# Optimization experiments

Hardware: AMD Instinct MI355X
Metric: run time of the kernel (lower is better)

## Reference

```python
import jax, jax.numpy as jnp
import numpy as np

B, S, D, H = 2, 2048, 1024, 16
DH = D // H  # 64
EPS = 1e-5


def setup_inputs() -> dict:
    key = jax.random.key(0)
    ks = jax.random.split(key, 16)
    s = 0.02
    return {
        "emb": jax.random.normal(ks[0], (B, S, D), dtype=jnp.float32),
        # per-head projections, stacked: torch Linear weight layout [out, in] -> [H, DH, D]
        "Wq": jax.random.normal(ks[1], (H, DH, D), dtype=jnp.float32) * s,
        "bq": jnp.zeros((H, DH), dtype=jnp.float32),
        "Wk": jax.random.normal(ks[2], (H, DH, D), dtype=jnp.float32) * s,
        "bk": jnp.zeros((H, DH), dtype=jnp.float32),
        "Wv": jax.random.normal(ks[3], (H, DH, D), dtype=jnp.float32) * s,
        "bv": jnp.zeros((H, DH), dtype=jnp.float32),
        "W0": jax.random.normal(ks[4], (D, D), dtype=jnp.float32) * s,
        "b0": jnp.zeros((D,), dtype=jnp.float32),
        "g1": jnp.ones((D,), dtype=jnp.float32),
        "be1": jnp.zeros((D,), dtype=jnp.float32),
        "W1": jax.random.normal(ks[5], (4 * D, D), dtype=jnp.float32) * s,
        "b1": jnp.zeros((4 * D,), dtype=jnp.float32),
        "W2": jax.random.normal(ks[6], (D, 4 * D), dtype=jnp.float32) * s,
        "b2": jnp.zeros((D,), dtype=jnp.float32),
        "g2": jnp.ones((D,), dtype=jnp.float32),
        "be2": jnp.zeros((D,), dtype=jnp.float32),
    }


def _layer_norm(x, g, b):
    mu = jnp.mean(x, axis=-1, keepdims=True)
    var = jnp.mean(jnp.square(x - mu), axis=-1, keepdims=True)
    return (x - mu) * jax.lax.rsqrt(var + EPS) * g + b


def reference(emb, Wq, bq, Wk, bk, Wv, bv, W0, b0, g1, be1, W1, b1, W2, b2, g2, be2):
    # per-head Q/K/V projections, batched over heads  -> [B, H, S, DH]
    q = jnp.einsum("bsd,hed->bhse", emb, Wq) + bq[None, :, None, :]
    k = jnp.einsum("bsd,hed->bhse", emb, Wk) + bk[None, :, None, :]
    v = jnp.einsum("bsd,hed->bhse", emb, Wv) + bv[None, :, None, :]
    # NOTE: original module applies NO scale before softmax; it divides the
    # softmax(QK^T) @ V output by sqrt(d_head) afterwards. Kept faithfully.
    scores = jnp.einsum("bhse,bhte->bhst", q, k)  # [B,H,S,S]
    attn = jax.nn.softmax(scores, axis=-1)
    z = jnp.einsum("bhst,bhte->bhse", attn, v) / np.sqrt(DH).astype(np.float32)
    # concat heads along feature dim (head 0 first) -> [B, S, D]
    z = z.transpose(0, 2, 1, 3).reshape(B, S, D)
    z = z @ W0.T + b0
    out1 = _layer_norm(z + emb, g1, be1)
    h = jax.nn.relu(out1 @ W1.T + b1)  # [B, S, 4D]
    out2 = _layer_norm(out1 + (h @ W2.T + b2), g2, be2)
    return out2
```

## Files before the change

kernel.cpp:

```cpp
#include <hip/hip_runtime.h>
#include <hip/hip_bf16.h>
#include <cstdint>
#include <cmath>

#define DEV __device__ __forceinline__

typedef float f32x4 __attribute__((ext_vector_type(4)));
typedef float f32x16 __attribute__((ext_vector_type(16)));
typedef __bf16 bf16x8 __attribute__((ext_vector_type(8)));
typedef unsigned short u16;
typedef u16 u16x8 __attribute__((ext_vector_type(8)));
typedef u16 u16x4 __attribute__((ext_vector_type(4)));

DEV u16 f2bf(float f) {
  union { float f; uint32_t u; } x{f};
  uint32_t r = x.u + 0x7FFFu + ((x.u >> 16) & 1u);
  return (u16)(r >> 16);
}

DEV void gl_lds16(const u16* g, u16* l) {
  __builtin_amdgcn_global_load_lds((const __attribute__((address_space(1))) void*)g,
                                   (__attribute__((address_space(3))) void*)l, 16, 0, 0);
}

__global__ __launch_bounds__(256) void k_cvt_all(
    const float* __restrict__ emb, const float* __restrict__ Wq,
    const float* __restrict__ Wk, const float* __restrict__ Wv,
    const float* __restrict__ W0, const float* __restrict__ W1,
    const float* __restrict__ W2,
    u16* __restrict__ embb, u16* __restrict__ Wqb, u16* __restrict__ Wkb,
    u16* __restrict__ Wvb, u16* __restrict__ W0b, u16* __restrict__ W1b,
    u16* __restrict__ W2b) {
  const int step = gridDim.x * blockDim.x;
  for (int i4 = blockIdx.x * blockDim.x + threadIdx.x; i4 < 4194304; i4 += step) {
    const int i = i4 * 4;
    const float* s; u16* d; int off;
    if (i < 4194304)       { s = emb; d = embb; off = 0; }
    else if (i < 5242880)  { s = Wq;  d = Wqb;  off = 4194304; }
    else if (i < 6291456)  { s = Wk;  d = Wkb;  off = 5242880; }
    else if (i < 7340032)  { s = Wv;  d = Wvb;  off = 6291456; }
    else if (i < 8388608)  { s = W0;  d = W0b;  off = 7340032; }
    else if (i < 12582912) { s = W1;  d = W1b;  off = 8388608; }
    else                   { s = W2;  d = W2b;  off = 12582912; }
    float4 v = *reinterpret_cast<const float4*>(s + (i - off));
    u16x4 o;
    o[0] = f2bf(v.x); o[1] = f2bf(v.y); o[2] = f2bf(v.z); o[3] = f2bf(v.w);
    *reinterpret_cast<u16x4*>(d + (i - off)) = o;
  }
}


template <int MODE>
DEV void gemm_core128(const u16* __restrict__ A, const u16* __restrict__ B,
                      const float* __restrict__ bias, const float* __restrict__ res,
                      void* __restrict__ C, int N, int K, int m0, int n0,
                      float oscale) {
  __shared__ u16 sA[2][128 * 32];
  __shared__ u16 sB[2][128 * 32];
  const int tid = threadIdx.x;
  const int w = tid >> 6, l = tid & 63;
  const int lr = l & 15, lg = l >> 4;
  const int wr = (w >> 1) * 64, wc = (w & 1) * 64;

  f32x4 acc[4][4] = {};

  const int nt = K >> 5;
  const int sr = w * 16 + (l >> 2);
  const int sc = (l & 3) * 8;

  auto stage = [&](int buf, int t) {
    const u16* ga = A + (size_t)(m0 + sr) * K + t * 32 + sc;
    const u16* gb = B + (size_t)(n0 + sr) * K + t * 32 + sc;
    gl_lds16(ga, &sA[buf][w * 512]);
    gl_lds16(ga + (size_t)64 * K, &sA[buf][2048 + w * 512]);
    gl_lds16(gb, &sB[buf][w * 512]);
    gl_lds16(gb + (size_t)64 * K, &sB[buf][2048 + w * 512]);
  };

  auto compute = [&](int buf) {
    bf16x8 af[4], bfr[4];
#pragma unroll
    for (int mf = 0; mf < 4; ++mf)
      af[mf] = *(const bf16x8*)&sA[buf][(wr + mf * 16 + lr) * 32 + lg * 8];
#pragma unroll
    for (int nf = 0; nf < 4; ++nf)
      bfr[nf] = *(const bf16x8*)&sB[buf][(wc + nf * 16 + lr) * 32 + lg * 8];
#pragma unroll
    for (int mf = 0; mf < 4; ++mf)
#pragma unroll
      for (int nf = 0; nf < 4; ++nf)
        acc[mf][nf] = __builtin_amdgcn_mfma_f32_16x16x32_bf16(af[mf], bfr[nf],
                                                              acc[mf][nf], 0, 0, 0);
  };

  stage(0, 0);
  __syncthreads();
  int cur = 0;
  for (int t = 0; t < nt - 1; ++t) {
    stage(cur ^ 1, t + 1);
    compute(cur);
    __syncthreads();
    cur ^= 1;
  }
  compute(cur);

#pragma unroll
  for (int nf = 0; nf < 4; ++nf) {
    const int col = n0 + wc + nf * 16 + lr;
    const float bv = bias[col];
#pragma unroll
    for (int mf = 0; mf < 4; ++mf) {
      const int row0 = m0 + wr + mf * 16 + lg * 4;
#pragma unroll
      for (int r = 0; r < 4; ++r) {
        float v = acc[mf][nf][r] + bv;
        if (MODE == 0) v *= oscale;
        if (MODE == 1) v = fmaxf(v, 0.0f);
        const size_t idx = (size_t)(row0 + r) * N + col;
        if (MODE == 2) ((float*)C)[idx] = v + res[idx];
        else ((u16*)C)[idx] = f2bf(v);
      }
    }
  }
}

template <int MODE>
DEV void gemm_core64(const u16* __restrict__ A, const u16* __restrict__ B,
                     const float* __restrict__ bias, const float* __restrict__ res,
                     void* __restrict__ C, int N, int K, int m0, int n0,
                     float oscale) {
  __shared__ u16 sA[2][64 * 32];
  __shared__ u16 sB[2][128 * 32];
  const int tid = threadIdx.x;
  const int w = tid >> 6, l = tid & 63;
  const int lr = l & 15, lg = l >> 4;
  const int wr = (w >> 1) * 32, wc = (w & 1) * 64;

  f32x4 acc[2][4] = {};

  const int nt = K >> 5;
  const int sr = w * 16 + (l >> 2);
  const int sc = (l & 3) * 8;

  auto stage = [&](int buf, int t) {
    gl_lds16(A + (size_t)(m0 + sr) * K + t * 32 + sc, &sA[buf][w * 512]);
    const u16* gb = B + (size_t)(n0 + sr) * K + t * 32 + sc;
    gl_lds16(gb, &sB[buf][w * 512]);
    gl_lds16(gb + (size_t)64 * K, &sB[buf][2048 + w * 512]);
  };

  auto compute = [&](int buf) {
    bf16x8 af[2], bfr[4];
#pragma unroll
    for (int mf = 0; mf < 2; ++mf)
      af[mf] = *(const bf16x8*)&sA[buf][(wr + mf * 16 + lr) * 32 + lg * 8];
#pragma unroll
    for (int nf = 0; nf < 4; ++nf)
      bfr[nf] = *(const bf16x8*)&sB[buf][(wc + nf * 16 + lr) * 32 + lg * 8];
#pragma unroll
    for (int mf = 0; mf < 2; ++mf)
#pragma unroll
      for (int nf = 0; nf < 4; ++nf)
        acc[mf][nf] = __builtin_amdgcn_mfma_f32_16x16x32_bf16(af[mf], bfr[nf],
                                                              acc[mf][nf], 0, 0, 0);
  };

  stage(0, 0);
  __syncthreads();
  int cur = 0;
  for (int t = 0; t < nt - 1; ++t) {
    stage(cur ^ 1, t + 1);
    compute(cur);
    __syncthreads();
    cur ^= 1;
  }
  compute(cur);

#pragma unroll
  for (int nf = 0; nf < 4; ++nf) {
    const int col = n0 + wc + nf * 16 + lr;
    const float bv = bias[col];
#pragma unroll
    for (int mf = 0; mf < 2; ++mf) {
      const int row0 = m0 + wr + mf * 16 + lg * 4;
#pragma unroll
      for (int r = 0; r < 4; ++r) {
        float v = acc[mf][nf][r] + bv;
        if (MODE == 0) v *= oscale;
        if (MODE == 1) v = fmaxf(v, 0.0f);
        const size_t idx = (size_t)(row0 + r) * N + col;
        if (MODE == 2) ((float*)C)[idx] = v + res[idx];
        else ((u16*)C)[idx] = f2bf(v);
      }
    }
  }
}

template <int MODE>
__global__ __launch_bounds__(256) void k_gemm(const u16* __restrict__ A,
                                              const u16* __restrict__ B,
                                              const float* __restrict__ bias,
                                              const float* __restrict__ res,
                                              void* __restrict__ C, int N, int K) {
  gemm_core128<MODE>(A, B, bias, res, C, N, K, blockIdx.x * 128, blockIdx.y * 128, 1.0f);
}

template <int MODE>
__global__ __launch_bounds__(256) void k_gemm64(const u16* __restrict__ A,
                                                const u16* __restrict__ B,
                                                const float* __restrict__ bias,
                                                const float* __restrict__ res,
                                                void* __restrict__ C, int N, int K) {
  gemm_core64<MODE>(A, B, bias, res, C, N, K, blockIdx.x * 64, blockIdx.y * 128, 1.0f);
}

__global__ __launch_bounds__(256) void k_gemm_qkv(
    const u16* __restrict__ A, const u16* __restrict__ B0, const u16* __restrict__ B1,
    const u16* __restrict__ B2, const float* __restrict__ c0,
    const float* __restrict__ c1, const float* __restrict__ c2,
    u16* __restrict__ O0, u16* __restrict__ O1, u16* __restrict__ O2) {
  const int z = blockIdx.z;
  const u16* B = (z == 0) ? B0 : (z == 1) ? B1 : B2;
  const float* bias = (z == 0) ? c0 : (z == 1) ? c1 : c2;
  u16* O = (z == 0) ? O0 : (z == 1) ? O1 : O2;
  const float sc = (z == 0) ? 1.44269504f : 1.0f;
  gemm_core64<0>(A, B, bias, nullptr, O, 1024, 1024, blockIdx.x * 64,
                 blockIdx.y * 128, sc);
}

__global__ __launch_bounds__(256, 4) void k_attn(const u16* __restrict__ Q,
                                                 const u16* __restrict__ K,
                                                 const u16* __restrict__ V,
                                                 float* __restrict__ pz,
                                                 float* __restrict__ pl) {
  const int id = blockIdx.x;
  const int virt = (id & 7) * 128 + (id >> 3);
  const int bh = virt >> 5;
  const int qt = (virt >> 1) & 15;
  const int half = virt & 1;
  const int b = bh >> 4, h = bh & 15;
  const int tid = threadIdx.x;
  const int w = tid >> 6, l = tid & 63;
  const int q32 = l & 31, hi = l >> 5;

  __shared__ u16 Kl[2][4096];
  __shared__ u16 VT[2][4096];

  const size_t rb = (size_t)b * 2048;
  const int c0 = h * 64;
  const int q0w = qt * 128 + w * 32;
  const int t0 = half * 16;

  bf16x8 qb[4];
#pragma unroll
  for (int st = 0; st < 4; ++st)
    qb[st] = *(const bf16x8*)(Q + (rb + q0w + q32) * 1024 + c0 + st * 16 + hi * 8);

  f32x16 zacc[2] = {};
  f32x4 lacc = {};

  const int skv = w * 16 + (l >> 3);
  const int sc8 = l & 7;
  auto stage_k = [&](int pp, int t) {
#pragma unroll
    for (int cq = 0; cq < 2; ++cq) {
      const int kvl = skv + cq * 8;
      const int dh0 = (sc8 ^ (kvl & 7)) * 8;
      gl_lds16(K + (rb + t * 64 + kvl) * 1024 + c0 + dh0,
               &Kl[pp][w * 1024 + cq * 512]);
    }
  };

  const int vp = tid & 31, vd0 = (tid >> 5) * 8;
  u16x8 va0, va1;
  auto vload = [&](int t) {
    const u16* v0 = V + (rb + t * 64 + 2 * vp) * 1024 + c0 + vd0;
    va0 = *(const u16x8*)v0;
    va1 = *(const u16x8*)(v0 + 1024);
  };
  auto vstore = [&](int pp) {
#pragma unroll
    for (int i = 0; i < 8; ++i) {
      const int dh = vd0 + i;
      const int off = ((2 * vp) & 7) + 8 * ((vp >> 2) ^ (dh & 7));
      uint32_t pk = (uint32_t)va0[i] | ((uint32_t)va1[i] << 16);
      *(uint32_t*)&VT[pp][dh * 64 + off] = pk;
    }
  };

  stage_k(0, t0);
  vload(t0);
  vstore(0);
  __syncthreads();

  for (int tt = 0; tt < 16; ++tt) {
    const int bp = tt & 1;
    if (tt + 1 < 16) {
      stage_k(bp ^ 1, t0 + tt + 1);
      vload(t0 + tt + 1);
    }
    f32x16 s[2] = {};
    __builtin_amdgcn_s_setprio(1);
#pragma unroll
    for (int nf = 0; nf < 2; ++nf)
#pragma unroll
      for (int st = 0; st < 4; ++st) {
        bf16x8 ka = *(const bf16x8*)&Kl[bp][(nf * 32 + q32) * 64 +
                                            ((st * 2 + hi) ^ (q32 & 7)) * 8];
        s[nf] = __builtin_amdgcn_mfma_f32_32x32x16_bf16(ka, qb[st], s[nf], 0, 0, 0);
      }
    __builtin_amdgcn_s_setprio(0);

    uint32_t c[16];
#pragma unroll
    for (int nf = 0; nf < 2; ++nf)
#pragma unroll
      for (int m2 = 0; m2 < 8; ++m2) {
        float p0 = exp2f(s[nf][2 * m2]);
        float p1 = exp2f(s[nf][2 * m2 + 1]);
        lacc[m2 & 3] += p0 + p1;
        uint32_t pk;
        asm("v_cvt_pk_bf16_f32 %0, %1, %2" : "=v"(pk) : "v"(p0), "v"(p1));
        c[nf * 8 + m2] = pk;
      }
#pragma unroll
    for (int ks = 0; ks < 4; ++ks) {
      asm("v_permlane32_swap_b32 %0, %1" : "+v"(c[4 * ks]), "+v"(c[4 * ks + 2]));
      asm("v_permlane32_swap_b32 %0, %1" : "+v"(c[4 * ks + 1]), "+v"(c[4 * ks + 3]));
    }

    if (tt + 1 < 16) vstore(bp ^ 1);

    __builtin_amdgcn_s_setprio(1);
#pragma unroll
    for (int ks = 0; ks < 4; ++ks) {
      union { uint32_t u[4]; bf16x8 v; } pa;
#pragma unroll
      for (int i = 0; i < 4; ++i) pa.u[i] = c[4 * ks + i];
#pragma unroll
      for (int nd = 0; nd < 2; ++nd) {
        bf16x8 vb = *(const bf16x8*)&VT[bp][(nd * 32 + q32) * 64 +
                                            ((ks * 2 + hi) ^ (q32 & 7)) * 8];
        zacc[nd] = __builtin_amdgcn_mfma_f32_32x32x16_bf16(pa.v, vb, zacc[nd], 0, 0, 0);
      }
    }
    __builtin_amdgcn_s_setprio(0);
    __syncthreads();
  }

  float* pzb = pz + (size_t)virt * 8192;
#pragma unroll
  for (int r = 0; r < 16; ++r) {
    const int crow = (r & 3) + 8 * (r >> 2) + 4 * hi;
#pragma unroll
    for (int nd = 0; nd < 2; ++nd)
      pzb[(w * 32 + crow) * 64 + nd * 32 + q32] = zacc[nd][r];
  }
  float lrun = (lacc[0] + lacc[1]) + (lacc[2] + lacc[3]);
  float ltot = lrun + __shfl_xor(lrun, 32, 64);
  if (hi == 0) pl[virt * 128 + w * 32 + q32] = ltot;
}

__global__ __launch_bounds__(256) void k_attn_merge(const float* __restrict__ pz,
                                                    const float* __restrict__ pl,
                                                    u16* __restrict__ Z) {
  const int id = blockIdx.x;
  const int virt2 = (id & 7) * 64 + (id >> 3);
  const int bh = virt2 >> 4, qt = virt2 & 15;
  const int b = bh >> 4, h = bh & 15;
  const int va = 2 * virt2;
  const int tid = threadIdx.x;
  const int row = tid >> 1;
  const int col0 = (tid & 1) * 32;

  const float la = pl[va * 128 + row];
  const float lb = pl[(va + 1) * 128 + row];
  const float inv = 0.125f / (la + lb);

  const float* za = pz + (size_t)va * 8192 + row * 64 + col0;
  const float* zb = za + 8192;
  u16* zo = Z + ((size_t)b * 2048 + qt * 128 + row) * 1024 + h * 64 + col0;
#pragma unroll
  for (int e = 0; e < 8; ++e) {
    float4 a = *(const float4*)(za + e * 4);
    float4 bv = *(const float4*)(zb + e * 4);
    u16x4 o;
    o[0] = f2bf((a.x + bv.x) * inv);
    o[1] = f2bf((a.y + bv.y) * inv);
    o[2] = f2bf((a.z + bv.z) * inv);
    o[3] = f2bf((a.w + bv.w) * inv);
    *(u16x4*)(zo + e * 4) = o;
  }
}

template <bool WBF>
__global__ __launch_bounds__(256) void k_ln(const float* __restrict__ x,
                                            const float* __restrict__ g,
                                            const float* __restrict__ be,
                                            float* __restrict__ of,
                                            u16* __restrict__ ob) {
  const int row = blockIdx.x;
  const int tid = threadIdx.x;
  const float* xr = x + (size_t)row * 1024;
  float4 v = *(const float4*)(xr + tid * 4);
  float s = v.x + v.y + v.z + v.w;
  float s2 = v.x * v.x + v.y * v.y + v.z * v.z + v.w * v.w;
#pragma unroll
  for (int st = 1; st < 64; st <<= 1) {
    s += __shfl_xor(s, st, 64);
    s2 += __shfl_xor(s2, st, 64);
  }
  __shared__ float ps[8];
  if ((tid & 63) == 0) { ps[tid >> 6] = s; ps[4 + (tid >> 6)] = s2; }
  __syncthreads();
  s = ps[0] + ps[1] + ps[2] + ps[3];
  s2 = ps[4] + ps[5] + ps[6] + ps[7];
  const float mu = s * 0.0009765625f;
  const float var = s2 * 0.0009765625f - mu * mu;
  const float rs = rsqrtf(var + 1e-5f);
  float4 gg = *(const float4*)(g + tid * 4);
  float4 bb = *(const float4*)(be + tid * 4);
  float4 o;
  o.x = (v.x - mu) * rs * gg.x + bb.x;
  o.y = (v.y - mu) * rs * gg.y + bb.y;
  o.z = (v.z - mu) * rs * gg.z + bb.z;
  o.w = (v.w - mu) * rs * gg.w + bb.w;
  *(float4*)(of + (size_t)row * 1024 + tid * 4) = o;
  if (WBF) {
    u16x4 q;
    q[0] = f2bf(o.x); q[1] = f2bf(o.y); q[2] = f2bf(o.z); q[3] = f2bf(o.w);
    *(u16x4*)(ob + (size_t)row * 1024 + tid * 4) = q;
  }
}

extern "C" void kernel_launch(void* const* d_in, const int* in_sizes, int n_in,
                              void* d_out, int out_size, void* d_ws, size_t ws_size,
                              hipStream_t stream) {
  const float* emb = (const float*)d_in[0];
  const float* Wq  = (const float*)d_in[1];
  const float* bq  = (const float*)d_in[2];
  const float* Wk  = (const float*)d_in[3];
  const float* bk  = (const float*)d_in[4];
  const float* Wv  = (const float*)d_in[5];
  const float* bv  = (const float*)d_in[6];
  const float* W0  = (const float*)d_in[7];
  const float* b0  = (const float*)d_in[8];
  const float* g1  = (const float*)d_in[9];
  const float* be1 = (const float*)d_in[10];
  const float* W1  = (const float*)d_in[11];
  const float* b1  = (const float*)d_in[12];
  const float* W2  = (const float*)d_in[13];
  const float* b2  = (const float*)d_in[14];
  const float* g2  = (const float*)d_in[15];
  const float* be2 = (const float*)d_in[16];

  char* p = (char*)d_ws;
  auto alloc = [&](size_t bytes) { char* r = p; p += bytes; return r; };
  u16* embb = (u16*)alloc(8u << 20);
  u16* Wqb  = (u16*)alloc(2u << 20);
  u16* Wkb  = (u16*)alloc(2u << 20);
  u16* Wvb  = (u16*)alloc(2u << 20);
  u16* W0b  = (u16*)alloc(2u << 20);
  u16* W1b  = (u16*)alloc(8u << 20);
  u16* W2b  = (u16*)alloc(8u << 20);
  u16* Qb   = (u16*)alloc(8u << 20);
  u16* Kb   = (u16*)alloc(8u << 20);
  u16* Vb   = (u16*)alloc(8u << 20);
  u16* Zb   = (u16*)alloc(8u << 20);
  float* y1 = (float*)alloc(16u << 20);
  float* o1f = (float*)alloc(16u << 20);
  u16* o1b  = (u16*)alloc(8u << 20);
  u16* hb   = (u16*)alloc(32u << 20);
  float* pl = (float*)alloc(1u << 20);

  float* pz = (float*)hb;

  k_cvt_all<<<2048, 256, 0, stream>>>(emb, Wq, Wk, Wv, W0, W1, W2,
                                      embb, Wqb, Wkb, Wvb, W0b, W1b, W2b);

  k_gemm_qkv<<<dim3(64, 8, 3), 256, 0, stream>>>(embb, Wqb, Wkb, Wvb, bq, bk, bv,
                                                 Qb, Kb, Vb);
  k_attn<<<dim3(1024), 256, 0, stream>>>(Qb, Kb, Vb, pz, pl);
  k_attn_merge<<<dim3(512), 256, 0, stream>>>(pz, pl, Zb);
  k_gemm64<2><<<dim3(64, 8), 256, 0, stream>>>(Zb, W0b, b0, emb, y1, 1024, 1024);
  k_ln<true><<<4096, 256, 0, stream>>>(y1, g1, be1, o1f, o1b);
  k_gemm64<1><<<dim3(64, 32), 256, 0, stream>>>(o1b, W1b, b1, nullptr, hb, 4096, 1024);
  k_gemm64<2><<<dim3(64, 8), 256, 0, stream>>>(hb, W2b, b2, o1f, y1, 1024, 4096);
  k_ln<false><<<4096, 256, 0, stream>>>(y1, g2, be2, (float*)d_out, nullptr);
}
```

Measured before the change: 309.5 us.

## Split-K the N=1024 GEMMs and fuse partial sum, bias, residual into LayerNorm

The two 1024-wide output GEMMs (attention output projection and FFN down projection) now run as split-K with two K halves, giving twice as many blocks (1024 instead of 512) to fill the GPU. Each half writes fp32 partials into reused scratch buffers, and the LayerNorm kernel now sums both partials plus bias and residual before normalizing. This trades extra fp32 partial traffic (two 16MB writes and reads per GEMM) for better occupancy, especially for the K=4096 GEMM. The unused 128-tile GEMM core is removed.

```diff
diff --git a/kernel.cpp b/kernel.cpp
--- a/kernel.cpp
+++ b/kernel.cpp
@@ -49,44 +49,41 @@
   }
 }
 
-
 template <int MODE>
-DEV void gemm_core128(const u16* __restrict__ A, const u16* __restrict__ B,
-                      const float* __restrict__ bias, const float* __restrict__ res,
-                      void* __restrict__ C, int N, int K, int m0, int n0,
-                      float oscale) {
-  __shared__ u16 sA[2][128 * 32];
+DEV void gemm_core64(const u16* __restrict__ A, const u16* __restrict__ B,
+                     const float* __restrict__ bias,
+                     void* __restrict__ C, int N, int K, int KL,
+                     int m0, int n0, float oscale) {
+  __shared__ u16 sA[2][64 * 32];
   __shared__ u16 sB[2][128 * 32];
   const int tid = threadIdx.x;
   const int w = tid >> 6, l = tid & 63;
   const int lr = l & 15, lg = l >> 4;
-  const int wr = (w >> 1) * 64, wc = (w & 1) * 64;
-
-  f32x4 acc[4][4] = {};
-
-  const int nt = K >> 5;
+  const int wr = (w >> 1) * 32, wc = (w & 1) * 64;
+
+  f32x4 acc[2][4] = {};
+
+  const int nt = KL >> 5;
   const int sr = w * 16 + (l >> 2);
   const int sc = (l & 3) * 8;
 
   auto stage = [&](int buf, int t) {
-    const u16* ga = A + (size_t)(m0 + sr) * K + t * 32 + sc;
+    gl_lds16(A + (size_t)(m0 + sr) * K + t * 32 + sc, &sA[buf][w * 512]);
     const u16* gb = B + (size_t)(n0 + sr) * K + t * 32 + sc;
-    gl_lds16(ga, &sA[buf][w * 512]);
-    gl_lds16(ga + (size_t)64 * K, &sA[buf][2048 + w * 512]);
     gl_lds16(gb, &sB[buf][w * 512]);
     gl_lds16(gb + (size_t)64 * K, &sB[buf][2048 + w * 512]);
   };
 
   auto compute = [&](int buf) {
-    bf16x8 af[4], bfr[4];
-#pragma unroll
-    for (int mf = 0; mf < 4; ++mf)
+    bf16x8 af[2], bfr[4];
+#pragma unroll
+    for (int mf = 0; mf < 2; ++mf)
       af[mf] = *(const bf16x8*)&sA[buf][(wr + mf * 16 + lr) * 32 + lg * 8];
 #pragma unroll
     for (int nf = 0; nf < 4; ++nf)
       bfr[nf] = *(const bf16x8*)&sB[buf][(wc + nf * 16 + lr) * 32 + lg * 8];
 #pragma unroll
-    for (int mf = 0; mf < 4; ++mf)
+    for (int mf = 0; mf < 2; ++mf)
 #pragma unroll
       for (int nf = 0; nf < 4; ++nf)
         acc[mf][nf] = __builtin_amdgcn_mfma_f32_16x16x32_bf16(af[mf], bfr[nf],
@@ -107,9 +104,9 @@
 #pragma unroll
   for (int nf = 0; nf < 4; ++nf) {
     const int col = n0 + wc + nf * 16 + lr;
-    const float bv = bias[col];
-#pragma unroll
-    for (int mf = 0; mf < 4; ++mf) {
+    const float bv = (MODE == 3) ? 0.0f : bias[col];
+#pragma unroll
+    for (int mf = 0; mf < 2; ++mf) {
       const int row0 = m0 + wr + mf * 16 + lg * 4;
 #pragma unroll
       for (int r = 0; r < 4; ++r) {
@@ -117,101 +114,29 @@
         if (MODE == 0) v *= oscale;
         if (MODE == 1) v = fmaxf(v, 0.0f);
         const size_t idx = (size_t)(row0 + r) * N + col;
-        if (MODE == 2) ((float*)C)[idx] = v + res[idx];
+        if (MODE == 3) ((float*)C)[idx] = v;
         else ((u16*)C)[idx] = f2bf(v);
       }
     }
   }
-}
-
-template <int MODE>
-DEV void gemm_core64(const u16* __restrict__ A, const u16* __restrict__ B,
-                     const float* __restrict__ bias, const float* __restrict__ res,
-                     void* __restrict__ C, int N, int K, int m0, int n0,
-                     float oscale) {
-  __shared__ u16 sA[2][64 * 32];
-  __shared__ u16 sB[2][128 * 32];
-  const int tid = threadIdx.x;
-  const int w = tid >> 6, l = tid & 63;
-  const int lr = l & 15, lg = l >> 4;
-  const int wr = (w >> 1) * 32, wc = (w & 1) * 64;
-
-  f32x4 acc[2][4] = {};
-
-  const int nt = K >> 5;
-  const int sr = w * 16 + (l >> 2);
-  const int sc = (l & 3) * 8;
-
-  auto stage = [&](int buf, int t) {
-    gl_lds16(A + (size_t)(m0 + sr) * K + t * 32 + sc, &sA[buf][w * 512]);
-    const u16* gb = B + (size_t)(n0 + sr) * K + t * 32 + sc;
-    gl_lds16(gb, &sB[buf][w * 512]);
-    gl_lds16(gb + (size_t)64 * K, &sB[buf][2048 + w * 512]);
-  };
-
-  auto compute = [&](int buf) {
-    bf16x8 af[2], bfr[4];
-#pragma unroll
-    for (int mf = 0; mf < 2; ++mf)
-      af[mf] = *(const bf16x8*)&sA[buf][(wr + mf * 16 + lr) * 32 + lg * 8];
-#pragma unroll
-    for (int nf = 0; nf < 4; ++nf)
-      bfr[nf] = *(const bf16x8*)&sB[buf][(wc + nf * 16 + lr) * 32 + lg * 8];
-#pragma unroll
-    for (int mf = 0; mf < 2; ++mf)
-#pragma unroll
-      for (int nf = 0; nf < 4; ++nf)
-        acc[mf][nf] = __builtin_amdgcn_mfma_f32_16x16x32_bf16(af[mf], bfr[nf],
-                                                              acc[mf][nf], 0, 0, 0);
-  };
-
-  stage(0, 0);
-  __syncthreads();
-  int cur = 0;
-  for (int t = 0; t < nt - 1; ++t) {
-    stage(cur ^ 1, t + 1);
-    compute(cur);
-    __syncthreads();
-    cur ^= 1;
-  }
-  compute(cur);
-
-#pragma unroll
-  for (int nf = 0; nf < 4; ++nf) {
-    const int col = n0 + wc + nf * 16 + lr;
-    const float bv = bias[col];
-#pragma unroll
-    for (int mf = 0; mf < 2; ++mf) {
-      const int row0 = m0 + wr + mf * 16 + lg * 4;
-#pragma unroll
-      for (int r = 0; r < 4; ++r) {
-        float v = acc[mf][nf][r] + bv;
-        if (MODE == 0) v *= oscale;
-        if (MODE == 1) v = fmaxf(v, 0.0f);
-        const size_t idx = (size_t)(row0 + r) * N + col;
-        if (MODE == 2) ((float*)C)[idx] = v + res[idx];
-        else ((u16*)C)[idx] = f2bf(v);
-      }
-    }
-  }
-}
-
-template <int MODE>
-__global__ __launch_bounds__(256) void k_gemm(const u16* __restrict__ A,
-                                              const u16* __restrict__ B,
-                                              const float* __restrict__ bias,
-                                              const float* __restrict__ res,
-                                              void* __restrict__ C, int N, int K) {
-  gemm_core128<MODE>(A, B, bias, res, C, N, K, blockIdx.x * 128, blockIdx.y * 128, 1.0f);
 }
 
 template <int MODE>
 __global__ __launch_bounds__(256) void k_gemm64(const u16* __restrict__ A,
                                                 const u16* __restrict__ B,
                                                 const float* __restrict__ bias,
-                                                const float* __restrict__ res,
                                                 void* __restrict__ C, int N, int K) {
-  gemm_core64<MODE>(A, B, bias, res, C, N, K, blockIdx.x * 64, blockIdx.y * 128, 1.0f);
+  gemm_core64<MODE>(A, B, bias, C, N, K, K, blockIdx.x * 64, blockIdx.y * 128, 1.0f);
+}
+
+__global__ __launch_bounds__(256) void k_gemm64sk(const u16* __restrict__ A,
+                                                  const u16* __restrict__ B,
+                                                  float* __restrict__ C,
+                                                  int N, int K, int Kh,
+                                                  size_t partStride) {
+  const int z = blockIdx.z;
+  gemm_core64<3>(A + z * Kh, B + z * Kh, nullptr, C + z * partStride,
+                 N, K, Kh, blockIdx.x * 64, blockIdx.y * 128, 1.0f);
 }
 
 __global__ __launch_bounds__(256) void k_gemm_qkv(
@@ -224,7 +149,7 @@
   const float* bias = (z == 0) ? c0 : (z == 1) ? c1 : c2;
   u16* O = (z == 0) ? O0 : (z == 1) ? O1 : O2;
   const float sc = (z == 0) ? 1.44269504f : 1.0f;
-  gemm_core64<0>(A, B, bias, nullptr, O, 1024, 1024, blockIdx.x * 64,
+  gemm_core64<0>(A, B, bias, O, 1024, 1024, 1024, blockIdx.x * 64,
                  blockIdx.y * 128, sc);
 }
 
@@ -394,15 +319,27 @@
 }
 
 template <bool WBF>
-__global__ __launch_bounds__(256) void k_ln(const float* __restrict__ x,
-                                            const float* __restrict__ g,
-                                            const float* __restrict__ be,
-                                            float* __restrict__ of,
-                                            u16* __restrict__ ob) {
+__global__ __launch_bounds__(256) void k_ln_merge(const float* __restrict__ pa,
+                                                  const float* __restrict__ pb,
+                                                  const float* __restrict__ bias,
+                                                  const float* __restrict__ res,
+                                                  const float* __restrict__ g,
+                                                  const float* __restrict__ be,
+                                                  float* __restrict__ of,
+                                                  u16* __restrict__ ob) {
   const int row = blockIdx.x;
   const int tid = threadIdx.x;
-  const float* xr = x + (size_t)row * 1024;
-  float4 v = *(const float4*)(xr + tid * 4);
+  const size_t base = (size_t)row * 1024 + tid * 4;
+  float4 a = *(const float4*)(pa + base);
+  float4 b = *(const float4*)(pb + base);
+  float4 rr = *(const float4*)(res + base);
+  float4 bv = *(const float4*)(bias + tid * 4);
+  float4 v;
+  v.x = a.x + b.x + rr.x + bv.x;
+  v.y = a.y + b.y + rr.y + bv.y;
+  v.z = a.z + b.z + rr.z + bv.z;
+  v.w = a.w + b.w + rr.w + bv.w;
+
   float s = v.x + v.y + v.z + v.w;
   float s2 = v.x * v.x + v.y * v.y + v.z * v.z + v.w * v.w;
 #pragma unroll
@@ -467,7 +404,6 @@
   u16* Kb   = (u16*)alloc(8u << 20);
   u16* Vb   = (u16*)alloc(8u << 20);
   u16* Zb   = (u16*)alloc(8u << 20);
-  float* y1 = (float*)alloc(16u << 20);
   float* o1f = (float*)alloc(16u << 20);
   u16* o1b  = (u16*)alloc(8u << 20);
   u16* hb   = (u16*)alloc(32u << 20);
@@ -482,9 +418,17 @@
                                                  Qb, Kb, Vb);
   k_attn<<<dim3(1024), 256, 0, stream>>>(Qb, Kb, Vb, pz, pl);
   k_attn_merge<<<dim3(512), 256, 0, stream>>>(pz, pl, Zb);
-  k_gemm64<2><<<dim3(64, 8), 256, 0, stream>>>(Zb, W0b, b0, emb, y1, 1024, 1024);
-  k_ln<true><<<4096, 256, 0, stream>>>(y1, g1, be1, o1f, o1b);
-  k_gemm64<1><<<dim3(64, 32), 256, 0, stream>>>(o1b, W1b, b1, nullptr, hb, 4096, 1024);
-  k_gemm64<2><<<dim3(64, 8), 256, 0, stream>>>(hb, W2b, b2, o1f, y1, 1024, 4096);
-  k_ln<false><<<4096, 256, 0, stream>>>(y1, g2, be2, (float*)d_out, nullptr);
-}
+
+  float* w0p = (float*)hb;
+  k_gemm64sk<<<dim3(64, 8, 2), 256, 0, stream>>>(Zb, W0b, w0p, 1024, 1024, 512,
+                                                 (size_t)4096 * 1024);
+  k_ln_merge<true><<<4096, 256, 0, stream>>>(w0p, w0p + (size_t)4096 * 1024,
+                                             b0, emb, g1, be1, o1f, o1b);
+  k_gemm64<1><<<dim3(64, 32), 256, 0, stream>>>(o1b, W1b, b1, hb, 4096, 1024);
+  float* f2p = (float*)Qb;
+  k_gemm64sk<<<dim3(64, 8, 2), 256, 0, stream>>>(hb, W2b, f2p, 1024, 4096, 2048,
+                                                 (size_t)4096 * 1024);
+  k_ln_merge<false><<<4096, 256, 0, stream>>>(f2p, f2p + (size_t)4096 * 1024,
+                                              b2, o1f, g2, be2, (float*)d_out,
+                                              nullptr);
+}
```

Measured after the change: 296.1 us. 1.05x faster.
